# Performance work log

Measured on AMD Instinct MI355X. Metric: run time of the kernel, lower is better.

Reference implementation:

```python
import jax, jax.numpy as jnp
import numpy as np

H_FEAT, W_FEAT, C_FEAT = 96, 96, 64
UP = 4
HQ, WQ = H_FEAT * UP, W_FEAT * UP
HID, DEPTH = 64, 2
MOD_DIM = HID * 2 * DEPTH          # scale + shift per hidden layer -> 256
HYP_IN = C_FEAT * 9 + 2            # unfolded feat + rel_cell -> 578
HYP_HID = 256


def make_coord(h, w):
    # pixel-center coords in [-1,1], order (y, x) matching (h, w)
    y = ((jnp.arange(h, dtype=jnp.float32) + 0.5) / h) * 2.0 - 1.0
    x = ((jnp.arange(w, dtype=jnp.float32) + 0.5) / w) * 2.0 - 1.0
    yy, xx = jnp.meshgrid(y, x, indexing='ij')
    return jnp.stack([yy, xx], axis=-1)  # (h, w, 2)


def _unfold3(feat):
    # F.unfold(feat, 3, padding=1).view(B, C*9, h, w): channel-major patch order
    B, C, h, w = feat.shape
    p = jnp.pad(feat, ((0, 0), (0, 0), (1, 1), (1, 1)))
    patches = jnp.stack([p[:, :, dy:dy + h, dx:dx + w]
                         for dy in range(3) for dx in range(3)], axis=2)
    return patches.reshape(B, C * 9, h, w)


def _gather_nearest(img, coord):
    # grid_sample(img, coord.flip(-1), mode='nearest', align_corners=False)
    # img: (B, C, H, W); coord: (B, Q, 2) in (y, x) order, range [-1, 1]
    B, C, H, W = img.shape
    iy = jnp.clip(jnp.round((coord[..., 0] + 1.0) * H / 2.0 - 0.5), 0, H - 1).astype(jnp.int32)
    ix = jnp.clip(jnp.round((coord[..., 1] + 1.0) * W / 2.0 - 0.5), 0, W - 1).astype(jnp.int32)
    idx = (iy * W + ix)[:, None, :]                      # (B, 1, Q)
    out = jnp.take_along_axis(img.reshape(B, C, H * W), idx, axis=2)
    return out.transpose(0, 2, 1)                        # (B, Q, C)


def setup_inputs() -> dict:
    key = jax.random.key(0)
    ks = jax.random.split(key, 6)
    s = 0.02
    feat = jax.random.normal(ks[0], (1, C_FEAT, H_FEAT, W_FEAT), jnp.float32)
    coord = make_coord(HQ, WQ).reshape(1, HQ * WQ, 2)
    cell = jnp.broadcast_to(jnp.array([2.0 / HQ, 2.0 / WQ], jnp.float32),
                            (1, HQ * WQ, 2)).astype(jnp.float32)
    return {
        'feat': feat, 'coord': coord, 'cell': cell,
        'Wh1': jax.random.normal(ks[1], (HYP_IN, HYP_HID), jnp.float32) * s,
        'bh1': jnp.zeros((HYP_HID,), jnp.float32),
        'Wh2': jax.random.normal(ks[2], (HYP_HID, MOD_DIM), jnp.float32) * s,
        'bh2': jnp.zeros((MOD_DIM,), jnp.float32),
        'W0': jax.random.normal(ks[3], (C_FEAT + 4, HID), jnp.float32) * s,
        'b0': jnp.zeros((HID,), jnp.float32),
        'W1': jax.random.normal(ks[4], (HID, HID), jnp.float32) * s,
        'b1': jnp.zeros((HID,), jnp.float32),
        'W2': jax.random.normal(ks[5], (HID, 3), jnp.float32) * s,
        'b2': jnp.zeros((3,), jnp.float32),
    }


def reference(feat, coord, cell, Wh1, bh1, Wh2, bh2, W0, b0, W1, b1, W2, b2):
    B, C, h, w = feat.shape
    hw_scale = jnp.array([h, w], jnp.float32)

    # --- gen_feats: 3x3 unfold for the hypernet input ---
    rich = _unfold3(feat)                                   # (B, 9C, h, w)

    # --- gen_modulations: per-latent-pixel hypernet MLP ---
    hyp_in = rich.transpose(0, 2, 3, 1).reshape(B, h * w, C * 9)
    rel_cell_lr = cell[:, :h * w, :] * hw_scale             # cell_decode
    hyp_in = jnp.concatenate([hyp_in, rel_cell_lr], axis=-1)
    mod = jax.nn.relu(hyp_in @ Wh1 + bh1) @ Wh2 + bh2       # (B, h*w, MOD_DIM)
    mod = mod.reshape(B, h, w, MOD_DIM).transpose(0, 3, 1, 2)

    feat_coord = jnp.broadcast_to(
        make_coord(h, w).transpose(2, 0, 1)[None], (B, 2, h, w))

    # --- query_rgb: local-ensemble gather -> modulated MLP -> area blend ---
    rx, ry = 1.0 / h, 1.0 / w                               # 2/h/2, 2/w/2
    eps = 1e-6
    rel_cell_q = cell * hw_scale                            # (B, Q, 2)
    preds, areas = [], []
    for vx in (-1.0, 1.0):
        for vy in (-1.0, 1.0):
            c_ = coord + jnp.array([vx * rx + eps, vy * ry + eps], jnp.float32)
            c_ = jnp.clip(c_, -1.0 + 1e-6, 1.0 - 1e-6)
            q_feat = _gather_nearest(feat, c_)              # (B, Q, C)
            q_coord = _gather_nearest(feat_coord, c_)       # (B, Q, 2)
            q_mod = _gather_nearest(mod, c_)                # (B, Q, MOD_DIM)
            rel = (coord - q_coord) * hw_scale              # (B, Q, 2)
            x = jnp.concatenate([q_feat, rel, rel_cell_q], axis=-1)
            # imnet: hidden layers modulated by (scale, shift) from hypernet
            x = x @ W0 + b0
            x = jax.nn.relu(x * q_mod[..., 0:HID] + q_mod[..., 2 * HID:3 * HID])
            x = x @ W1 + b1
            x = jax.nn.relu(x * q_mod[..., HID:2 * HID] + q_mod[..., 3 * HID:4 * HID])
            preds.append(x @ W2 + b2)                       # (B, Q, 3)
            areas.append(jnp.abs(rel[..., 0] * rel[..., 1]) + 1e-9)

    # diagonal-swap of ensemble areas (LIIF local ensemble)
    areas[0], areas[3] = areas[3], areas[0]
    areas[1], areas[2] = areas[2], areas[1]
    tot = areas[0] + areas[1] + areas[2] + areas[3]
    out = sum(p * (a / tot)[..., None] for p, a in zip(preds, areas))
    return out  # (B, Q, 3)
```

## Files before the change

kernel.cpp:

```cpp
#include <hip/hip_runtime.h>


#define HW 96
#define NPIX (96*96)
#define CFEAT 64
#define INV192 (1.0f/192.0f)

typedef __attribute__((ext_vector_type(8))) short short8;
typedef __attribute__((ext_vector_type(4))) float f32x4;

__device__ __forceinline__ unsigned pack_bf2(float a, float b) {
    unsigned ua = __builtin_bit_cast(unsigned, a);
    unsigned ub = __builtin_bit_cast(unsigned, b);
    return (ua >> 16) | (ub & 0xffff0000u);
}
__device__ __forceinline__ float bf_hi(float a) {
    return __builtin_bit_cast(float, __builtin_bit_cast(unsigned, a) & 0xffff0000u);
}
__device__ __forceinline__ void split8(const float (&v)[8], short8& hi, short8& lo) {
    union { short8 s; unsigned u[4]; } H, L;
    #pragma unroll
    for (int p = 0; p < 4; ++p) {
        float a = v[2*p], b = v[2*p+1];
        H.u[p] = pack_bf2(a, b);
        L.u[p] = pack_bf2(a - bf_hi(a), b - bf_hi(b));
    }
    hi = H.s; lo = L.s;
}
__device__ __forceinline__ unsigned rne16(float x) {
    unsigned u = __builtin_bit_cast(unsigned, x);
    return (u + 0x7fffu + ((u >> 16) & 1u)) >> 16;
}
__device__ __forceinline__ unsigned pack_bf2_rne(float a, float b) {
    return rne16(a) | (rne16(b) << 16);
}
__device__ __forceinline__ short top16(float a) {
    return (short)(__builtin_bit_cast(unsigned, a) >> 16);
}

__device__ __forceinline__ float dpp_red16(float v) {
    int x;
    x = __builtin_amdgcn_update_dpp(0, __builtin_bit_cast(int, v), 0xB1, 0xF, 0xF, true);
    v += __builtin_bit_cast(float, x);
    x = __builtin_amdgcn_update_dpp(0, __builtin_bit_cast(int, v), 0x4E, 0xF, 0xF, true);
    v += __builtin_bit_cast(float, x);
    x = __builtin_amdgcn_update_dpp(0, __builtin_bit_cast(int, v), 0x141, 0xF, 0xF, true);
    v += __builtin_bit_cast(float, x);
    x = __builtin_amdgcn_update_dpp(0, __builtin_bit_cast(int, v), 0x140, 0xF, 0xF, true);
    v += __builtin_bit_cast(float, x);
    return v;
}

#define AXCALC(CV, SGN, II, RR)                                        \
{                                                                      \
    float e = CV + (SGN)*(1.0f/96.0f) + 1e-6f;                         \
    e = fminf(fmaxf(e, -1.0f + 1e-6f), 1.0f - 1e-6f);                  \
    II = (int)rintf((e + 1.0f) * 48.0f - 0.5f);                        \
    II = min(max(II, 0), 95);                                          \
    RR = (CV - fmaf((float)II, 0.0208333333f, -0.9895833333f)) * 96.0f;\
}

__global__ __launch_bounds__(256) void swizzle_kernel(
    const float* __restrict__ Wh1, const float* __restrict__ Wh2,
    const float* __restrict__ W0, const float* __restrict__ W1,
    short* __restrict__ wsw)
{
    const int gid = blockIdx.x*256 + threadIdx.x;
    if (gid >= 432*64) return;
    const int f    = gid >> 6;
    const int lane = gid & 63;
    const int c    = lane & 15;
    const int kg   = lane >> 4;
    const float* W; int kt, nt, N;
    if (f < 288)      { W = Wh1; kt = f >> 4;        nt = f & 15;        N = 256; }
    else if (f < 416) { W = Wh2; kt = (f-288) >> 4;  nt = (f-288) & 15;  N = 256; }
    else if (f < 424) { W = W0;  kt = (f-416) >> 2;  nt = (f-416) & 3;   N = 64;  }
    else              { W = W1;  kt = (f-424) >> 2;  nt = (f-424) & 3;   N = 64;  }
    union { short8 s; unsigned u[4]; } H;
    #pragma unroll
    for (int p = 0; p < 4; ++p) {
        float a = W[(kt*32 + kg*8 + 2*p    )*N + nt*16 + c];
        float b = W[(kt*32 + kg*8 + 2*p + 1)*N + nt*16 + c];
        H.u[p] = pack_bf2_rne(a, b);
    }
    *(short8*)(wsw + (size_t)f*512 + lane*8) = H.s;
}

__global__ __launch_bounds__(512) void hyper_mfma(
    const float* __restrict__ feat,
    const float* __restrict__ cell,
    const float* __restrict__ Wh1,
    const float* __restrict__ bh1,
    const float* __restrict__ bh2,
    const float* __restrict__ b0,
    const short* __restrict__ wsw,
    float* __restrict__ mod_ws,
    float* __restrict__ f0_ws)
{
    __shared__ short AHI[72*128];
    __shared__ short ALO[72*128];
    __shared__ short HHI[32*128];
    __shared__ short HLO[32*128];

    const int tid = threadIdx.x;
    const int blk = blockIdx.x;
    const int y   = blk / 6;
    const int x0  = (blk % 6) * 16;
    const int qbase = y*HW + x0;

    for (int idx = tid; idx < 9216; idx += 512) {
        const int px = idx & 15;
        const int k  = idx >> 4;
        const int ch = k / 9;
        const int j  = k - 9*ch;
        const int dy = j / 3;
        const int dx = j - 3*dy;
        const int gy = y + dy - 1;
        const int gx = x0 + px + dx - 1;
        float v = 0.0f;
        if (gy >= 0 && gy < HW && gx >= 0 && gx < HW)
            v = feat[ch*NPIX + gy*HW + gx];
        const int dst = (k >> 3)*128 + px*8 + (k & 7);
        AHI[dst] = top16(v);
        ALO[dst] = top16(v - bf_hi(v));
    }
    __syncthreads();

    const int lane = tid & 63;
    const int wid  = tid >> 6;
    const int c    = lane & 15;
    const int kg   = lane >> 4;

    const short* wh1f = wsw;
    const short* wh2f = wsw + (size_t)288*512;
    const short* w0f  = wsw + (size_t)416*512;

    if (wid < 4) {
        f32x4 acc0;
        const float bb = b0[wid*16 + c];
        acc0[0] = bb; acc0[1] = bb; acc0[2] = bb; acc0[3] = bb;
        #pragma unroll
        for (int kt = 0; kt < 2; ++kt) {
            float v[8];
            #pragma unroll
            for (int j = 0; j < 8; ++j)
                v[j] = feat[(kt*32 + kg*8 + j)*NPIX + y*HW + x0 + c];
            short8 Ahi, Alo;
            split8(v, Ahi, Alo);
            const short8 B = *(const short8*)(w0f + (size_t)(kt*4 + wid)*512 + lane*8);
            acc0 = __builtin_amdgcn_mfma_f32_16x16x32_bf16(Ahi, B, acc0, 0, 0, 0);
            acc0 = __builtin_amdgcn_mfma_f32_16x16x32_bf16(Alo, B, acc0, 0, 0, 0);
        }
        #pragma unroll
        for (int i = 0; i < 4; ++i)
            f0_ws[(size_t)(qbase + kg*4 + i)*64 + wid*16 + c] = acc0[i];
    }

    f32x4 acc[2];
    #pragma unroll
    for (int nt = 0; nt < 2; ++nt) {
        const float bb = bh1[wid*32 + nt*16 + c];
        acc[nt][0] = bb; acc[nt][1] = bb; acc[nt][2] = bb; acc[nt][3] = bb;
    }
    #pragma unroll
    for (int kt = 0; kt < 18; ++kt) {
        const int aoff = (kt*4 + kg)*128 + c*8;
        const short8 Ahi = *(const short8*)&AHI[aoff];
        const short8 Alo = *(const short8*)&ALO[aoff];
        #pragma unroll
        for (int nt = 0; nt < 2; ++nt) {
            const short8 B = *(const short8*)(wh1f + (size_t)(kt*16 + wid*2 + nt)*512 + lane*8);
            acc[nt] = __builtin_amdgcn_mfma_f32_16x16x32_bf16(Ahi, B, acc[nt], 0, 0, 0);
            acc[nt] = __builtin_amdgcn_mfma_f32_16x16x32_bf16(Alo, B, acc[nt], 0, 0, 0);
        }
    }
    {
        float rc0v[4], rc1v[4];
        #pragma unroll
        for (int i = 0; i < 4; ++i) {
            const int q = qbase + kg*4 + i;
            const float2 ce = ((const float2*)cell)[q];
            rc0v[i] = ce.x * 96.0f;
            rc1v[i] = ce.y * 96.0f;
        }
        #pragma unroll
        for (int nt = 0; nt < 2; ++nt) {
            const int n = wid*32 + nt*16 + c;
            const float w5 = Wh1[576*256 + n];
            const float w6 = Wh1[577*256 + n];
            #pragma unroll
            for (int i = 0; i < 4; ++i) {
                float hv = acc[nt][i] + rc0v[i]*w5 + rc1v[i]*w6;
                hv = fmaxf(hv, 0.0f);
                const int dst = (n >> 3)*128 + (kg*4 + i)*8 + (n & 7);
                HHI[dst] = top16(hv);
                HLO[dst] = top16(hv - bf_hi(hv));
            }
        }
    }
    __syncthreads();

    f32x4 acc2[2];
    #pragma unroll
    for (int nt = 0; nt < 2; ++nt) {
        const float bb = bh2[wid*32 + nt*16 + c];
        acc2[nt][0] = bb; acc2[nt][1] = bb; acc2[nt][2] = bb; acc2[nt][3] = bb;
    }
    #pragma unroll
    for (int kt = 0; kt < 8; ++kt) {
        const int aoff = (kt*4 + kg)*128 + c*8;
        const short8 Ahi = *(const short8*)&HHI[aoff];
        const short8 Alo = *(const short8*)&HLO[aoff];
        #pragma unroll
        for (int nt = 0; nt < 2; ++nt) {
            const short8 B = *(const short8*)(wh2f + (size_t)(kt*16 + wid*2 + nt)*512 + lane*8);
            acc2[nt] = __builtin_amdgcn_mfma_f32_16x16x32_bf16(Ahi, B, acc2[nt], 0, 0, 0);
            acc2[nt] = __builtin_amdgcn_mfma_f32_16x16x32_bf16(Alo, B, acc2[nt], 0, 0, 0);
        }
    }
    #pragma unroll
    for (int nt = 0; nt < 2; ++nt) {
        #pragma unroll
        for (int i = 0; i < 4; ++i)
            mod_ws[(size_t)(qbase + kg*4 + i)*256 + wid*32 + nt*16 + c] = acc2[nt][i];
    }
}

#define ROWQ 324

__global__ __launch_bounds__(256) void query_kernel_v8(
    const float* __restrict__ cell,
    const float* __restrict__ W0,
    const short* __restrict__ wsw,
    const float* __restrict__ b1,
    const float* __restrict__ W2,
    const float* __restrict__ b2,
    const float* __restrict__ mod_ws,
    const float* __restrict__ f0_ws,
    float* __restrict__ out)
{
    __shared__ float smem[24*ROWQ];

    const int tid = threadIdx.x;
    const int bX  = blockIdx.x % 48;
    const int bY  = blockIdx.x / 48;
    const int X0  = bX * 8;
    const int Y0  = bY * 16;
    const int lx0 = bX*2 - 1;
    const int ly0 = bY*4 - 1;

    const float rc0 = cell[0] * 96.0f;
    const float rc1 = cell[1] * 96.0f;

    const float4* w64p = (const float4*)(W0 + 64*64);
    const float4* w65p = (const float4*)(W0 + 65*64);
    const float4* w66p = (const float4*)(W0 + 66*64);
    const float4* w67p = (const float4*)(W0 + 67*64);

    for (int idx = tid; idx < 1536; idx += 256) {
        const int r  = idx >> 6;
        const int o  = idx & 63;
        const int ry = r >> 2;
        const int rx = r & 3;
        const int gy = min(max(ly0 + ry, 0), 95);
        const int gx = min(max(lx0 + rx, 0), 95);
        const int src = gy*96 + gx;
        const float4* modv = (const float4*)(mod_ws + (size_t)src*256);
        if (o < 16) {
            const float4 f0 = ((const float4*)(f0_ws + (size_t)src*64))[o];
            const float4 s1 = modv[o];
            const float4 t1 = modv[32 + o];
            const float4 a  = w66p[o];
            const float4 b  = w67p[o];
            float4 v;
            v.x = fmaf(s1.x, fmaf(rc1, b.x, fmaf(rc0, a.x, f0.x)), t1.x);
            v.y = fmaf(s1.y, fmaf(rc1, b.y, fmaf(rc0, a.y, f0.y)), t1.y);
            v.z = fmaf(s1.z, fmaf(rc1, b.z, fmaf(rc0, a.z, f0.z)), t1.z);
            v.w = fmaf(s1.w, fmaf(rc1, b.w, fmaf(rc0, a.w, f0.w)), t1.w);
            *(float4*)(smem + r*ROWQ + o*4) = v;
        } else if (o < 32) {
            const int oo = o - 16;
            const float4 s1 = modv[oo];
            const float4 w  = w64p[oo];
            float4 v = {s1.x*w.x, s1.y*w.y, s1.z*w.z, s1.w*w.w};
            *(float4*)(smem + r*ROWQ + 64 + oo*4) = v;
        } else if (o < 48) {
            const int oo = o - 32;
            const float4 s1 = modv[oo];
            const float4 w  = w65p[oo];
            float4 v = {s1.x*w.x, s1.y*w.y, s1.z*w.z, s1.w*w.w};
            *(float4*)(smem + r*ROWQ + 128 + oo*4) = v;
        } else {
            const int oo = o - 48;
            const float4 s2 = modv[16 + oo];
            const float4 h2 = modv[48 + oo];
            #pragma unroll
            for (int j = 0; j < 4; ++j) {
                const int col = oo*4 + j;
                const int cc  = col & 15;
                const int nt  = col >> 4;
                const float sv = (j==0)?s2.x:(j==1)?s2.y:(j==2)?s2.z:s2.w;
                const float hv = (j==0)?h2.x:(j==1)?h2.y:(j==2)?h2.z:h2.w;
                smem[r*ROWQ + 192 + cc*4 + nt] = sv;
                smem[r*ROWQ + 256 + cc*4 + nt] = hv;
            }
        }
    }

    const int lane = tid & 63;
    const int wid  = tid >> 6;
    const int c    = lane & 15;
    const int kg   = lane >> 4;

    const short* w1f = wsw + (size_t)424*512;
    short8 Bh[4][2];
    #pragma unroll
    for (int kt = 0; kt < 2; ++kt)
        #pragma unroll
        for (int nt = 0; nt < 4; ++nt)
            Bh[nt][kt] = *(const short8*)(w1f + (size_t)(kt*4 + nt)*512 + lane*8);

    float b1c[4];
    float w2r[4][3];
    #pragma unroll
    for (int nt = 0; nt < 4; ++nt) {
        b1c[nt] = b1[nt*16 + c];
        w2r[nt][0] = W2[(nt*16 + c)*3 + 0];
        w2r[nt][1] = W2[(nt*16 + c)*3 + 1];
        w2r[nt][2] = W2[(nt*16 + c)*3 + 2];
    }
    const float b2v0 = b2[0], b2v1 = b2[1], b2v2 = b2[2];

    __syncthreads();

    const int Xw   = X0 + (wid & 1)*4;
    const int Yw   = Y0 + (wid >> 1)*8;
    const int qxA  = c >> 2;
    const int tapA = c & 3;
    const float vxA = (tapA < 2) ? -1.0f : 1.0f;
    const float vyA = (tapA & 1) ? 1.0f : -1.0f;

    const float cxA = ((float)(Xw + qxA) + 0.5f) * INV192 - 1.0f;
    const float cxE = ((float)(Xw + kg)  + 0.5f) * INV192 - 1.0f;
    int ixA; float r1A;
    AXCALC(cxA, vyA, ixA, r1A)
    const int ixAc = ixA - lx0;
    int ixm, ixp; float r1m, r1p;
    AXCALC(cxE, -1.0f, ixm, r1m)
    AXCALC(cxE,  1.0f, ixp, r1p)

    #pragma unroll 4
    for (int m = 0; m < 8; ++m) {
        const int qy = Yw + m;
        const float cy = ((float)qy + 0.5f) * INV192 - 1.0f;

        int iym, iyp; float r0m, r0p;
        AXCALC(cy, -1.0f, iym, r0m)
        AXCALC(cy,  1.0f, iyp, r0p)
        const int rym = (iym - ly0)*4 - lx0;
        const int ryp = (iyp - ly0)*4 - lx0;
        const int lr0 = rym + ixm, lr1 = rym + ixp;
        const int lr2 = ryp + ixm, lr3 = ryp + ixp;
        float4 sc2v[4], sh2v[4];
        #pragma unroll
        for (int i = 0; i < 4; ++i) {
            const int lri = (i == 0) ? lr0 : (i == 1) ? lr1 : (i == 2) ? lr2 : lr3;
            sc2v[i] = *(const float4*)(smem + lri*ROWQ + 192 + c*4);
            sh2v[i] = *(const float4*)(smem + lri*ROWQ + 256 + c*4);
        }
        const float a0 = fabsf(r0m*r1m) + 1e-9f;
        const float a1 = fabsf(r0m*r1p) + 1e-9f;
        const float a2 = fabsf(r0p*r1m) + 1e-9f;
        const float a3 = fabsf(r0p*r1p) + 1e-9f;
        const float invt = 1.0f / (a0 + a1 + a2 + a3);
        const float w0_ = a3 * invt, w1_ = a2 * invt, w2_ = a1 * invt, w3_ = a0 * invt;

        short8 A[2];
        {
            int iyA; float r0A;
            AXCALC(cy, vxA, iyA, r0A)
            const float* rowp = smem + ((iyA - ly0)*4 + ixAc) * ROWQ;
            #pragma unroll
            for (int kt = 0; kt < 2; ++kt) {
                const int kb = kt*32 + kg*8;
                const float4 ga  = *(const float4*)(rowp + kb);
                const float4 gb  = *(const float4*)(rowp + kb + 4);
                const float4 u0a = *(const float4*)(rowp + 64  + kb);
                const float4 u0b = *(const float4*)(rowp + 64  + kb + 4);
                const float4 u1a = *(const float4*)(rowp + 128 + kb);
                const float4 u1b = *(const float4*)(rowp + 128 + kb + 4);
                float g[8]  = {ga.x,ga.y,ga.z,ga.w,gb.x,gb.y,gb.z,gb.w};
                float u0[8] = {u0a.x,u0a.y,u0a.z,u0a.w,u0b.x,u0b.y,u0b.z,u0b.w};
                float u1[8] = {u1a.x,u1a.y,u1a.z,u1a.w,u1b.x,u1b.y,u1b.z,u1b.w};
                float hv[8];
                #pragma unroll
                for (int j = 0; j < 8; ++j) {
                    float pre = fmaf(r0A, u0[j], g[j]);
                    pre = fmaf(r1A, u1[j], pre);
                    hv[j] = fmaxf(pre, 0.f);
                }
                union { short8 s; unsigned u[4]; } P;
                #pragma unroll
                for (int p = 0; p < 4; ++p)
                    P.u[p] = pack_bf2_rne(hv[2*p], hv[2*p+1]);
                A[kt] = P.s;
            }
        }

        f32x4 acc[4];
        #pragma unroll
        for (int nt = 0; nt < 4; ++nt) {
            f32x4 z = {b1c[nt], b1c[nt], b1c[nt], b1c[nt]};
            acc[nt] = z;
        }
        #pragma unroll
        for (int nt = 0; nt < 4; ++nt) {
            #pragma unroll
            for (int kt = 0; kt < 2; ++kt)
                acc[nt] = __builtin_amdgcn_mfma_f32_16x16x32_bf16(A[kt], Bh[nt][kt], acc[nt], 0, 0, 0);
        }

        float p0 = 0.f, p1 = 0.f, p2 = 0.f;
        #pragma unroll
        for (int i = 0; i < 4; ++i) {
            const float wi = (i == 0) ? w0_ : (i == 1) ? w1_ : (i == 2) ? w2_ : w3_;
            float s0 = 0.f, s1 = 0.f, s2 = 0.f;
            #pragma unroll
            for (int nt = 0; nt < 4; ++nt) {
                const float sc2 = (nt==0)?sc2v[i].x:(nt==1)?sc2v[i].y:(nt==2)?sc2v[i].z:sc2v[i].w;
                const float sh2 = (nt==0)?sh2v[i].x:(nt==1)?sh2v[i].y:(nt==2)?sh2v[i].z:sh2v[i].w;
                const float v = fmaxf(fmaf(acc[nt][i], sc2, sh2), 0.f);
                s0 = fmaf(v, w2r[nt][0], s0);
                s1 = fmaf(v, w2r[nt][1], s1);
                s2 = fmaf(v, w2r[nt][2], s2);
            }
            p0 = fmaf(s0, wi, p0);
            p1 = fmaf(s1, wi, p1);
            p2 = fmaf(s2, wi, p2);
        }
        p0 = dpp_red16(p0);
        p1 = dpp_red16(p1);
        p2 = dpp_red16(p2);
        if (c < 3) {
            const int qE = qy*384 + Xw + kg;
            const float ov = (c == 0) ? p0 + b2v0 : (c == 1) ? p1 + b2v1 : p2 + b2v2;
            out[(size_t)qE*3 + c] = ov;
        }
    }
}

extern "C" void kernel_launch(void* const* d_in, const int* in_sizes, int n_in,
                              void* d_out, int out_size, void* d_ws, size_t ws_size,
                              hipStream_t stream) {
    const float* feat  = (const float*)d_in[0];
    const float* cell  = (const float*)d_in[2];
    const float* Wh1   = (const float*)d_in[3];
    const float* bh1   = (const float*)d_in[4];
    const float* Wh2   = (const float*)d_in[5];
    const float* bh2   = (const float*)d_in[6];
    const float* W0    = (const float*)d_in[7];
    const float* b0    = (const float*)d_in[8];
    const float* W1    = (const float*)d_in[9];
    const float* b1    = (const float*)d_in[10];
    const float* W2    = (const float*)d_in[11];
    const float* b2    = (const float*)d_in[12];
    float* out = (float*)d_out;

    float* mod_ws = (float*)d_ws;
    float* f0_ws  = (float*)d_ws + 9216*256;
    short* wsw    = (short*)((char*)d_ws + 11796480);

    swizzle_kernel<<<dim3(108), dim3(256), 0, stream>>>(Wh1, Wh2, W0, W1, wsw);
    hyper_mfma<<<dim3(576), dim3(512), 0, stream>>>(
        feat, cell, Wh1, bh1, bh2, b0, wsw, mod_ws, f0_ws);
    query_kernel_v8<<<dim3(1152), dim3(256), 0, stream>>>(
        cell, W0, wsw, b1, W2, b2, mod_ws, f0_ws, out);
}
```

Before: 76.73 us.

## Store query-stage layer-1 tables as bf16 in LDS and halve tile height

The per-pixel layer-1 tables (g, u0, u1) in shared memory are now stored as bf16 instead of fp32, and the scale/shift table moves to a separate smaller fp32 array. Each block covers 8 query rows instead of 16, which halves the halo rows staged and doubles the grid to 2304 blocks. The goal is less LDS use and fewer LDS reads per query, which should allow more resident blocks and better load balance. In exchange, the layer-1 pre-activation inputs lose precision through bf16 rounding, and staging overhead per output pixel goes up because the halo is relatively larger.

```diff
diff --git a/kernel.cpp b/kernel.cpp
--- a/kernel.cpp
+++ b/kernel.cpp
@@ -36,6 +36,12 @@
 }
 __device__ __forceinline__ short top16(float a) {
     return (short)(__builtin_bit_cast(unsigned, a) >> 16);
+}
+__device__ __forceinline__ float bf_lo_f(unsigned w) {
+    return __builtin_bit_cast(float, w << 16);
+}
+__device__ __forceinline__ float bf_hi_f(unsigned w) {
+    return __builtin_bit_cast(float, w & 0xffff0000u);
 }
 
 __device__ __forceinline__ float dpp_red16(float v) {
@@ -226,9 +232,10 @@
     }
 }
 
-#define ROWQ 324
-
-__global__ __launch_bounds__(256) void query_kernel_v8(
+#define ROWB 200
+#define ROWF 132
+
+__global__ __launch_bounds__(256) void query_kernel_v9(
     const float* __restrict__ cell,
     const float* __restrict__ W0,
     const short* __restrict__ wsw,
@@ -239,15 +246,16 @@
     const float* __restrict__ f0_ws,
     float* __restrict__ out)
 {
-    __shared__ float smem[24*ROWQ];
+    __shared__ short smemB[16*ROWB];
+    __shared__ float smemF[16*ROWF];
 
     const int tid = threadIdx.x;
     const int bX  = blockIdx.x % 48;
     const int bY  = blockIdx.x / 48;
     const int X0  = bX * 8;
-    const int Y0  = bY * 16;
+    const int Y0  = bY * 8;
     const int lx0 = bX*2 - 1;
-    const int ly0 = bY*4 - 1;
+    const int ly0 = bY*2 - 1;
 
     const float rc0 = cell[0] * 96.0f;
     const float rc1 = cell[1] * 96.0f;
@@ -257,7 +265,7 @@
     const float4* w66p = (const float4*)(W0 + 66*64);
     const float4* w67p = (const float4*)(W0 + 67*64);
 
-    for (int idx = tid; idx < 1536; idx += 256) {
+    for (int idx = tid; idx < 1024; idx += 256) {
         const int r  = idx >> 6;
         const int o  = idx & 63;
         const int ry = r >> 2;
@@ -272,24 +280,26 @@
             const float4 t1 = modv[32 + o];
             const float4 a  = w66p[o];
             const float4 b  = w67p[o];
-            float4 v;
-            v.x = fmaf(s1.x, fmaf(rc1, b.x, fmaf(rc0, a.x, f0.x)), t1.x);
-            v.y = fmaf(s1.y, fmaf(rc1, b.y, fmaf(rc0, a.y, f0.y)), t1.y);
-            v.z = fmaf(s1.z, fmaf(rc1, b.z, fmaf(rc0, a.z, f0.z)), t1.z);
-            v.w = fmaf(s1.w, fmaf(rc1, b.w, fmaf(rc0, a.w, f0.w)), t1.w);
-            *(float4*)(smem + r*ROWQ + o*4) = v;
+            float gx_ = fmaf(s1.x, fmaf(rc1, b.x, fmaf(rc0, a.x, f0.x)), t1.x);
+            float gy_ = fmaf(s1.y, fmaf(rc1, b.y, fmaf(rc0, a.y, f0.y)), t1.y);
+            float gz_ = fmaf(s1.z, fmaf(rc1, b.z, fmaf(rc0, a.z, f0.z)), t1.z);
+            float gw_ = fmaf(s1.w, fmaf(rc1, b.w, fmaf(rc0, a.w, f0.w)), t1.w);
+            uint2 pw = { pack_bf2_rne(gx_, gy_), pack_bf2_rne(gz_, gw_) };
+            *(uint2*)(smemB + r*ROWB + o*4) = pw;
         } else if (o < 32) {
             const int oo = o - 16;
             const float4 s1 = modv[oo];
             const float4 w  = w64p[oo];
-            float4 v = {s1.x*w.x, s1.y*w.y, s1.z*w.z, s1.w*w.w};
-            *(float4*)(smem + r*ROWQ + 64 + oo*4) = v;
+            uint2 pw = { pack_bf2_rne(s1.x*w.x, s1.y*w.y),
+                         pack_bf2_rne(s1.z*w.z, s1.w*w.w) };
+            *(uint2*)(smemB + r*ROWB + 64 + oo*4) = pw;
         } else if (o < 48) {
             const int oo = o - 32;
             const float4 s1 = modv[oo];
             const float4 w  = w65p[oo];
-            float4 v = {s1.x*w.x, s1.y*w.y, s1.z*w.z, s1.w*w.w};
-            *(float4*)(smem + r*ROWQ + 128 + oo*4) = v;
+            uint2 pw = { pack_bf2_rne(s1.x*w.x, s1.y*w.y),
+                         pack_bf2_rne(s1.z*w.z, s1.w*w.w) };
+            *(uint2*)(smemB + r*ROWB + 128 + oo*4) = pw;
         } else {
             const int oo = o - 48;
             const float4 s2 = modv[16 + oo];
@@ -301,8 +311,8 @@
                 const int nt  = col >> 4;
                 const float sv = (j==0)?s2.x:(j==1)?s2.y:(j==2)?s2.z:s2.w;
                 const float hv = (j==0)?h2.x:(j==1)?h2.y:(j==2)?h2.z:h2.w;
-                smem[r*ROWQ + 192 + cc*4 + nt] = sv;
-                smem[r*ROWQ + 256 + cc*4 + nt] = hv;
+                smemF[r*ROWF + cc*4 + nt]      = sv;
+                smemF[r*ROWF + 64 + cc*4 + nt] = hv;
             }
         }
     }
@@ -334,7 +344,7 @@
     __syncthreads();
 
     const int Xw   = X0 + (wid & 1)*4;
-    const int Yw   = Y0 + (wid >> 1)*8;
+    const int Yw   = Y0 + (wid >> 1)*4;
     const int qxA  = c >> 2;
     const int tapA = c & 3;
     const float vxA = (tapA < 2) ? -1.0f : 1.0f;
@@ -350,7 +360,7 @@
     AXCALC(cxE,  1.0f, ixp, r1p)
 
     #pragma unroll 4
-    for (int m = 0; m < 8; ++m) {
+    for (int m = 0; m < 4; ++m) {
         const int qy = Yw + m;
         const float cy = ((float)qy + 0.5f) * INV192 - 1.0f;
 
@@ -365,8 +375,8 @@
         #pragma unroll
         for (int i = 0; i < 4; ++i) {
             const int lri = (i == 0) ? lr0 : (i == 1) ? lr1 : (i == 2) ? lr2 : lr3;
-            sc2v[i] = *(const float4*)(smem + lri*ROWQ + 192 + c*4);
-            sh2v[i] = *(const float4*)(smem + lri*ROWQ + 256 + c*4);
+            sc2v[i] = *(const float4*)(smemF + lri*ROWF + c*4);
+            sh2v[i] = *(const float4*)(smemF + lri*ROWF + 64 + c*4);
         }
         const float a0 = fabsf(r0m*r1m) + 1e-9f;
         const float a1 = fabsf(r0m*r1p) + 1e-9f;
@@ -379,30 +389,24 @@
         {
             int iyA; float r0A;
             AXCALC(cy, vxA, iyA, r0A)
-            const float* rowp = smem + ((iyA - ly0)*4 + ixAc) * ROWQ;
+            const short* rowb = smemB + ((iyA - ly0)*4 + ixAc) * ROWB;
             #pragma unroll
             for (int kt = 0; kt < 2; ++kt) {
                 const int kb = kt*32 + kg*8;
-                const float4 ga  = *(const float4*)(rowp + kb);
-                const float4 gb  = *(const float4*)(rowp + kb + 4);
-                const float4 u0a = *(const float4*)(rowp + 64  + kb);
-                const float4 u0b = *(const float4*)(rowp + 64  + kb + 4);
-                const float4 u1a = *(const float4*)(rowp + 128 + kb);
-                const float4 u1b = *(const float4*)(rowp + 128 + kb + 4);
-                float g[8]  = {ga.x,ga.y,ga.z,ga.w,gb.x,gb.y,gb.z,gb.w};
-                float u0[8] = {u0a.x,u0a.y,u0a.z,u0a.w,u0b.x,u0b.y,u0b.z,u0b.w};
-                float u1[8] = {u1a.x,u1a.y,u1a.z,u1a.w,u1b.x,u1b.y,u1b.z,u1b.w};
-                float hv[8];
-                #pragma unroll
-                for (int j = 0; j < 8; ++j) {
-                    float pre = fmaf(r0A, u0[j], g[j]);
-                    pre = fmaf(r1A, u1[j], pre);
-                    hv[j] = fmaxf(pre, 0.f);
-                }
+                union { short8 s; unsigned u[4]; } GW, U0, U1;
+                GW.s = *(const short8*)(rowb + kb);
+                U0.s = *(const short8*)(rowb + 64 + kb);
+                U1.s = *(const short8*)(rowb + 128 + kb);
                 union { short8 s; unsigned u[4]; } P;
                 #pragma unroll
-                for (int p = 0; p < 4; ++p)
-                    P.u[p] = pack_bf2_rne(hv[2*p], hv[2*p+1]);
+                for (int p = 0; p < 4; ++p) {
+                    float g0 = bf_lo_f(GW.u[p]), g1 = bf_hi_f(GW.u[p]);
+                    float a0_ = bf_lo_f(U0.u[p]), a1_ = bf_hi_f(U0.u[p]);
+                    float b0_ = bf_lo_f(U1.u[p]), b1_ = bf_hi_f(U1.u[p]);
+                    float h0 = fmaxf(fmaf(r1A, b0_, fmaf(r0A, a0_, g0)), 0.f);
+                    float h1 = fmaxf(fmaf(r1A, b1_, fmaf(r0A, a1_, g1)), 0.f);
+                    P.u[p] = pack_bf2_rne(h0, h1);
+                }
                 A[kt] = P.s;
             }
         }
@@ -473,6 +477,6 @@
     swizzle_kernel<<<dim3(108), dim3(256), 0, stream>>>(Wh1, Wh2, W0, W1, wsw);
     hyper_mfma<<<dim3(576), dim3(512), 0, stream>>>(
         feat, cell, Wh1, bh1, bh2, b0, wsw, mod_ws, f0_ws);
-    query_kernel_v8<<<dim3(1152), dim3(256), 0, stream>>>(
+    query_kernel_v9<<<dim3(2304), dim3(256), 0, stream>>>(
         cell, W0, wsw, b1, W2, b2, mod_ws, f0_ws, out);
 }
```

Result: slower. 79.34 us (+3.4%).
